# Optimization experiments

Hardware: AMD Instinct MI355X
Metric: run time of the kernel (lower is better)

## Reference

```python
import jax, jax.numpy as jnp
import numpy as np

MIN_, MAX_, KSZ, IGNORE_IDX = 10, 10, 3, -255
B, H, W = 256, 256, 256
LI_MAX_ITERS = 64


def setup_inputs() -> dict:
    key = jax.random.key(0)
    x = jax.random.uniform(key, (B, 1, H, W), dtype=jnp.float32)
    return {"x": x}


def _otsu(hist):
    # hist: [256] counts. Returns Otsu threshold (bin value); fg = img > t.
    bins = jnp.arange(256, dtype=jnp.float32)
    w0 = jnp.cumsum(hist)[:-1]
    w1 = hist.sum() - w0
    s0 = jnp.cumsum(hist * bins)[:-1]
    s_tot = (hist * bins).sum()
    m0 = s0 / jnp.maximum(w0, 1e-12)
    m1 = (s_tot - s0) / jnp.maximum(w1, 1e-12)
    var_b = w0 * w1 * (m0 - m1) ** 2
    return jnp.argmax(var_b).astype(jnp.float32)


def _li(hist, init_t):
    # Histogram-based Li iterative minimum cross-entropy threshold
    # (skimage.filters.threshold_li with initial_guess=init_t).
    bins = jnp.arange(256, dtype=jnp.float32)
    img_min = jnp.min(jnp.where(hist > 0, bins, 255.0))
    vals = bins - img_min  # shift so values >= 0 (as skimage does)
    csum = jnp.cumsum(hist)
    cvsum = jnp.cumsum(hist * vals)
    n_tot, s_tot = csum[-1], cvsum[-1]
    tol = 0.5  # integer image -> half the minimal value spacing

    def body(state):
        t_curr, _, i = state
        # background: img <= t_curr + img_min
        idx = jnp.clip(jnp.floor(t_curr + img_min).astype(jnp.int32), 0, 255)
        n_back, s_back = csum[idx], cvsum[idx]
        n_fore, s_fore = n_tot - n_back, s_tot - s_back
        mean_back = jnp.where(n_back > 0, s_back / jnp.maximum(n_back, 1.0), 0.0)
        mean_fore = s_fore / jnp.maximum(n_fore, 1.0)
        eps = 1e-12
        t_next = (mean_back - mean_fore) / (
            jnp.log(jnp.maximum(mean_back, eps)) - jnp.log(jnp.maximum(mean_fore, eps)))
        t_next = jnp.where(mean_back < eps, mean_fore / 2.0, t_next)
        return (t_next, t_curr, i + 1)

    def cond(state):
        t_curr, t_prev, i = state
        return (jnp.abs(t_curr - t_prev) > tol) & (i < LI_MAX_ITERS)

    t0 = init_t - img_min
    t_fin, _, _ = jax.lax.while_loop(cond, body, (t0, t0 + 10.0, 0))
    return t_fin + img_min


def _sample_mask(key, region, k):
    # Uniform sampling without replacement of up to k pixels from region
    # (bool [H,W]) via random-score top-k (equiv. to torch.multinomial
    # with uniform probs, w/o replacement).
    flat = region.reshape(-1)
    scores = jnp.where(flat, jax.random.uniform(key, (flat.shape[0],)), -1.0)
    top, idx = jax.lax.top_k(scores, k)
    valid = (top >= 0.0).astype(jnp.int32)
    mask = jnp.zeros(flat.shape[0], jnp.int32).at[idx].max(valid)
    return mask.reshape(region.shape)


def _dilate(m):
    # kornia dilation with ones (KSZ,KSZ) kernel on a 0/1 mask == max filter.
    return jax.lax.reduce_window(m, 0, jax.lax.max, (KSZ, KSZ), (1, 1), "SAME")


def _per_image(img_u8, key_fg, key_bg):
    # img_u8: [H,W] int32 in [0,255]
    hist = jnp.zeros(256, jnp.float32).at[img_u8.ravel()].add(1.0)
    otsu = jnp.clip(_otsu(hist), 1.0, 254.0)  # clamp 0->1, 255->254
    li_t = _li(hist, otsu)
    roi = img_u8.astype(jnp.float32) > li_t

    fg = _sample_mask(key_fg, roi, MAX_)
    bg = _sample_mask(key_bg, jnp.logical_not(roi), MIN_)
    if KSZ > 1:
        fg = _dilate(fg)
        bg = _dilate(bg)

    overlap = (fg + bg) == 2
    fg = jnp.where(overlap, 0, fg)
    bg = jnp.where(overlap, 0, bg)

    seeds = jnp.full((H, W), IGNORE_IDX, jnp.int32)
    seeds = jnp.where(bg == 1, 0, seeds)
    seeds = jnp.where(fg == 1, 1, seeds)
    return seeds


def reference(x):
    b = x.shape[0]
    # (cam*255).astype(uint8): truncation, cam in [0,1]
    img = jnp.clip(jnp.floor(x[:, 0] * 255.0), 0, 255).astype(jnp.int32)
    keys = jax.random.split(jax.random.key(1), (b, 2))
    return jax.vmap(_per_image)(img, keys[:, 0], keys[:, 1])
```

## Files before the change

kernel.cpp:

```cpp
#include <hip/hip_runtime.h>
#include <stdint.h>

#define NPIX 65536
#define IGN (-255)
#define CAP 768

__device__ __forceinline__ uint32_t rotl32(uint32_t v, uint32_t r){ return (v<<r)|(v>>(32u-r)); }

__device__ __forceinline__ void tf2x32(uint32_t k0, uint32_t k1, uint32_t x0, uint32_t x1,
                                       uint32_t &o0, uint32_t &o1){
  uint32_t k2 = k0 ^ k1 ^ 0x1BD11BDAu;
  x0 += k0; x1 += k1;
#define TFR(r) { x0 += x1; x1 = rotl32(x1,(r)); x1 ^= x0; }
  TFR(13u) TFR(15u) TFR(26u) TFR(6u)   x0 += k1; x1 += k2 + 1u;
  TFR(17u) TFR(29u) TFR(16u) TFR(24u)  x0 += k2; x1 += k0 + 2u;
  TFR(13u) TFR(15u) TFR(26u) TFR(6u)   x0 += k0; x1 += k1 + 3u;
  TFR(17u) TFR(29u) TFR(16u) TFR(24u)  x0 += k1; x1 += k2 + 4u;
  TFR(13u) TFR(15u) TFR(26u) TFR(6u)   x0 += k2; x1 += k0 + 5u;
#undef TFR
  o0 = x0; o1 = x1;
}

__device__ __forceinline__ void tf2_pair(uint32_t A0, uint32_t A1, uint32_t xA,
                                         uint32_t B0, uint32_t B1, uint32_t xB,
                                         uint32_t &rA, uint32_t &rB){
  uint32_t A2 = A0 ^ A1 ^ 0x1BD11BDAu;
  uint32_t B2 = B0 ^ B1 ^ 0x1BD11BDAu;
  uint32_t a0 = A0, a1 = xA + A1;
  uint32_t b0 = B0, b1 = xB + B1;
#define TFR2(r) { a0 += a1; b0 += b1; a1 = rotl32(a1,(r)); b1 = rotl32(b1,(r)); a1 ^= a0; b1 ^= b0; }
  TFR2(13u) TFR2(15u) TFR2(26u) TFR2(6u)
  a0 += A1; b0 += B1; a1 += A2 + 1u; b1 += B2 + 1u;
  TFR2(17u) TFR2(29u) TFR2(16u) TFR2(24u)
  a0 += A2; b0 += B2; a1 += A0 + 2u; b1 += B0 + 2u;
  TFR2(13u) TFR2(15u) TFR2(26u) TFR2(6u)
  a0 += A0; b0 += B0; a1 += A1 + 3u; b1 += B1 + 3u;
  TFR2(17u) TFR2(29u) TFR2(16u) TFR2(24u)
  a0 += A1; b0 += B1; a1 += A2 + 4u; b1 += B2 + 4u;
  TFR2(13u) TFR2(15u) TFR2(26u) TFR2(6u)
  a0 += A2; b0 += B2; a1 += A0 + 5u; b1 += B0 + 5u;
#undef TFR2
  rA = a0 ^ a1; rB = b0 ^ b1;
}

__device__ __forceinline__ unsigned long long packCand(uint32_t bits, uint32_t pix){
  float f = __uint_as_float((bits >> 9) | 0x3f800000u) - 1.0f;
  uint32_t u = __float_as_uint(f) ^ 0x80000000u;
  return ((unsigned long long)u << 32) | (unsigned long long)(0xFFFFFFFFu - pix);
}

__device__ __forceinline__ void t10_insert(unsigned long long* l, unsigned long long c){
  if (c > l[9]) {
    l[9] = c;
#pragma unroll
    for (int i = 9; i > 0; --i){
      unsigned long long a = l[i-1], b2 = l[i];
      if (b2 > a){ l[i-1] = b2; l[i] = a; }
    }
  }
}

__global__ __launch_bounds__(1024)
void apm_kernel(const float* __restrict__ x, int* __restrict__ out){
  const int b = blockIdx.x;
  const int tid = threadIdx.x;
  const float* img = x + (size_t)b * NPIX;
  int* outb = out + (size_t)b * NPIX;

  __shared__ uint32_t histR[1024];
  __shared__ float csum[256], cvsum[256];
  __shared__ uint32_t s_kw[4];
  __shared__ unsigned long long buf[2][CAP];
  __shared__ int s_cnt[2], s_fail[2], s_np[2];
  __shared__ int s_qthr, s_nroi;
  __shared__ unsigned long long s_top[2][64][10];
  __shared__ unsigned long long s_top2[2][8][10];
  __shared__ int s_pr[2][10], s_pc[2][10];

  histR[tid] = 0u;
  if (tid < 2){
    uint32_t o0, o1;
    tf2x32(0u, 1u, 0u, (uint32_t)(2*b + tid), o0, o1);
    s_kw[2*tid] = o0; s_kw[2*tid+1] = o1;
    s_cnt[tid] = 0;
  }
  __syncthreads();

  {
    const float4* x4 = (const float4*)img;
    int4* o4 = (int4*)outb;
    const int4 f4 = make_int4(IGN, IGN, IGN, IGN);
    const uint32_t c4 = (uint32_t)(tid & 3);
    for (int k = 0; k < 16; ++k){
      int i4 = tid + 1024*k;
      float4 v = x4[i4];
      uint32_t u0 = (uint32_t)min(max((int)floorf(v.x*255.0f),0),255);
      uint32_t u1 = (uint32_t)min(max((int)floorf(v.y*255.0f),0),255);
      uint32_t u2 = (uint32_t)min(max((int)floorf(v.z*255.0f),0),255);
      uint32_t u3 = (uint32_t)min(max((int)floorf(v.w*255.0f),0),255);
      outb[i4] = (int)(u0 | (u1<<8) | (u2<<16) | (u3<<24));
      if (i4 >= 4096) o4[i4] = f4;
      atomicAdd(&histR[(u0<<2)|c4],1u); atomicAdd(&histR[(u1<<2)|c4],1u);
      atomicAdd(&histR[(u2<<2)|c4],1u); atomicAdd(&histR[(u3<<2)|c4],1u);
    }
  }
  __syncthreads();

  if (tid < 64){
    const int lane = tid;
    const int4* hv = (const int4*)&histR[16*lane];
    int4 p0 = hv[0], p1 = hv[1], p2 = hv[2], p3 = hv[3];
    int h0 = p0.x + p0.y + p0.z + p0.w;
    int h1 = p1.x + p1.y + p1.z + p1.w;
    int h2 = p2.x + p2.y + p2.z + p2.w;
    int h3 = p3.x + p3.y + p3.z + p3.w;
    int cand = 256;
    if (h3) cand = 4*lane + 3;
    if (h2) cand = 4*lane + 2;
    if (h1) cand = 4*lane + 1;
    if (h0) cand = 4*lane + 0;
    for (int off = 32; off; off >>= 1) cand = min(cand, __shfl_xor(cand, off));
    const float img_min = (float)cand;
    float c0 = (float)h0, c1 = c0 + h1, c2 = c1 + h2, c3 = c2 + h3;
    float bv = 4.0f*lane - img_min;
    float v0 = h0*bv;
    float v1 = v0 + h1*(bv + 1.0f);
    float v2 = v1 + h2*(bv + 2.0f);
    float v3 = v2 + h3*(bv + 3.0f);
    float cc = c3, vv = v3;
    for (int off = 1; off < 64; off <<= 1){
      float a = __shfl_up(cc, off), b2 = __shfl_up(vv, off);
      if (lane >= off){ cc += a; vv += b2; }
    }
    const float cexc = cc - c3, vexc = vv - v3;
    const float cs0 = cexc+c0, cs1 = cexc+c1, cs2 = cexc+c2, cs3 = cexc+c3;
    const float vs0 = vexc+v0, vs1 = vexc+v1, vs2 = vexc+v2, vs3 = vexc+v3;
    csum[4*lane]   = cs0; csum[4*lane+1]  = cs1;
    csum[4*lane+2] = cs2; csum[4*lane+3]  = cs3;
    cvsum[4*lane]   = vs0; cvsum[4*lane+1] = vs1;
    cvsum[4*lane+2] = vs2; cvsum[4*lane+3] = vs3;
    const float ctot = __shfl(cc, 63), vtot = __shfl(vv, 63);
    const float s_tot_o = vtot + img_min * ctot;
    unsigned long long best = 0ull;
#define OTSU_BIN(CS, VS, J)                                              \
    { int bin = 4*lane + (J);                                            \
      if (bin < 255){                                                    \
        float w0_ = (CS);                                                \
        float w1_ = 65536.0f - w0_;                                      \
        float cs = (VS) + img_min * (CS);                                \
        float m0 = cs / fmaxf(w0_, 1e-12f);                              \
        float m1 = (s_tot_o - cs) / fmaxf(w1_, 1e-12f);                  \
        float d = m0 - m1;                                               \
        float vb = (w0_*w1_) * (d*d);                                    \
        unsigned long long pk =                                          \
          ((unsigned long long)__float_as_uint(vb) << 32) |              \
           (unsigned long long)(255 - bin);                              \
        if (pk > best) best = pk;                                        \
      } }
    OTSU_BIN(cs0, vs0, 0) OTSU_BIN(cs1, vs1, 1)
    OTSU_BIN(cs2, vs2, 2) OTSU_BIN(cs3, vs3, 3)
#undef OTSU_BIN
    for (int off = 32; off; off >>= 1){
      unsigned int hi = (unsigned int)(best >> 32), lo = (unsigned int)best;
      unsigned int hio = (unsigned int)__shfl_xor((int)hi, off);
      unsigned int loo = (unsigned int)__shfl_xor((int)lo, off);
      unsigned long long ob = ((unsigned long long)hio << 32) | loo;
      if (ob > best) best = ob;
    }
    if (lane == 0){
      int bestIdx = 255 - (int)(best & 0xFFFFFFFFull);
      float otsu = fminf(fmaxf((float)bestIdx, 1.0f), 254.0f);
      float n_tot = ctot, s_tot = vtot;
      float t_curr = otsu - img_min, t_prev = t_curr + 10.0f;
      int it = 0;
      while (fabsf(t_curr - t_prev) > 0.5f && it < 64){
        int idx = min(max((int)floorf(t_curr + img_min), 0), 255);
        float n_back = csum[idx], s_back = cvsum[idx];
        float n_fore = n_tot - n_back, s_fore = s_tot - s_back;
        float mean_back = (n_back > 0.0f) ? (s_back / fmaxf(n_back, 1.0f)) : 0.0f;
        float mean_fore = s_fore / fmaxf(n_fore, 1.0f);
        float t_next = (mean_back - mean_fore) /
                       (logf(fmaxf(mean_back, 1e-12f)) - logf(fmaxf(mean_fore, 1e-12f)));
        if (mean_back < 1e-12f) t_next = mean_fore * 0.5f;
        t_prev = t_curr; t_curr = t_next; ++it;
      }
      float lit = t_curr + img_min;
      int qthr;
      if (!(lit == lit)) qthr = 256;
      else               qthr = (int)floorf(lit) + 1;
      s_qthr = qthr;
      int nlo = (qthr <= 0) ? 0 : (int)csum[min(qthr, 256) - 1];
      s_nroi = NPIX - nlo;
    }
  }
  __syncthreads();

  const int qthr = s_qthr;
  const uint32_t fk0 = s_kw[0], fk1 = s_kw[1], bk0 = s_kw[2], bk1 = s_kw[3];
  const int4* u4 = (const int4*)outb;
  for (int k = 0; k < 4; ++k){
    int4 w = u4[tid + 1024*k];
    uint32_t pw0 = (uint32_t)(16*(tid + 1024*k));
#pragma unroll
    for (int m = 0; m < 4; ++m){
      uint32_t pk = (m==0)?(uint32_t)w.x:(m==1)?(uint32_t)w.y:(m==2)?(uint32_t)w.z:(uint32_t)w.w;
      uint32_t pb = pw0 + (uint32_t)(4*m);
#pragma unroll
      for (int h = 0; h < 2; ++h){
        int qa = (int)((pk >> (16*h))     & 255u);
        int qb = (int)((pk >> (16*h + 8)) & 255u);
        bool ra = (qa >= qthr), rb = (qb >= qthr);
        uint32_t pixA = pb + (uint32_t)(2*h), pixB = pixA + 1u;
        uint32_t bitsA, bitsB;
        tf2_pair(ra ? fk0 : bk0, ra ? fk1 : bk1, pixA,
                 rb ? fk0 : bk0, rb ? fk1 : bk1, pixB, bitsA, bitsB);
        if (bitsA >= 0xFF000000u){
          int r2 = ra ? 0 : 1;
          int idx = atomicAdd(&s_cnt[r2], 1);
          if (idx < CAP) buf[r2][idx] = packCand(bitsA, pixA);
        }
        if (bitsB >= 0xFF000000u){
          int r2 = rb ? 0 : 1;
          int idx = atomicAdd(&s_cnt[r2], 1);
          if (idx < CAP) buf[r2][idx] = packCand(bitsB, pixB);
        }
      }
    }
  }
  __syncthreads();

  if (tid < 2){
    int rs = tid ? (NPIX - s_nroi) : s_nroi;
    int cc = s_cnt[tid];
    s_fail[tid] = (cc > CAP) || (cc < 10 && cc != rs);
  }
  __syncthreads();

  const int wv = tid >> 6, lane = tid & 63;
  if (wv < 2){
    const int r2 = wv;
    unsigned long long t[10];
#pragma unroll
    for (int i = 0; i < 10; ++i) t[i] = 0ull;
    if (!s_fail[r2]){
      int n = min(s_cnt[r2], CAP);
      for (int i = lane; i < n; i += 64) t10_insert(t, buf[r2][i]);
    } else {
      const uint32_t kk0 = s_kw[2*r2], kk1 = s_kw[2*r2+1];
      for (int k = 0; k < 1024; ++k){
        uint32_t pix = (uint32_t)(lane + 64*k);
        int q = (int)(((uint32_t)outb[pix >> 2] >> (8*(pix & 3u))) & 255u);
        bool r = (q >= qthr);
        if (r == (r2 == 0)){
          uint32_t o0, o1; tf2x32(kk0, kk1, 0u, pix, o0, o1);
          t10_insert(t, packCand(o0 ^ o1, pix));
        }
      }
    }
#pragma unroll
    for (int i = 0; i < 10; ++i) s_top[r2][lane][i] = t[i];
  }
  __syncthreads();
  if (wv < 2 && lane < 8){
    unsigned long long t[10];
#pragma unroll
    for (int i = 0; i < 10; ++i) t[i] = 0ull;
    for (int l2 = 0; l2 < 8; ++l2)
#pragma unroll
      for (int i = 0; i < 10; ++i) t10_insert(t, s_top[wv][lane*8 + l2][i]);
#pragma unroll
    for (int i = 0; i < 10; ++i) s_top2[wv][lane][i] = t[i];
  }
  __syncthreads();
  if (wv < 2 && lane == 0){
    unsigned long long t[10];
#pragma unroll
    for (int i = 0; i < 10; ++i) t[i] = 0ull;
    for (int l2 = 0; l2 < 8; ++l2)
#pragma unroll
      for (int i = 0; i < 10; ++i) t10_insert(t, s_top2[wv][l2][i]);
    int np = 0;
    for (int i = 0; i < 10; ++i){
      if (t[i]){
        uint32_t pix = 0xFFFFFFFFu - (uint32_t)(t[i] & 0xFFFFFFFFull);
        s_pr[wv][np] = (int)(pix >> 8);
        s_pc[wv][np] = (int)(pix & 255u);
        ++np;
      }
    }
    s_np[wv] = np;
  }
  __syncthreads();

  {
    int4* o4 = (int4*)outb;
    const int4 f4 = make_int4(IGN, IGN, IGN, IGN);
#pragma unroll
    for (int k = 0; k < 4; ++k) o4[tid + 1024*k] = f4;
  }
  __syncthreads();

  const int nfg = s_np[0], nbg = s_np[1];
  const int npts = nfg + nbg;
  if (tid < npts*9){
    int k = tid / 9, d = tid - k*9;
    int pr = (k < nfg) ? s_pr[0][k] : s_pr[1][k - nfg];
    int pc = (k < nfg) ? s_pc[0][k] : s_pc[1][k - nfg];
    pr += d/3 - 1; pc += d%3 - 1;
    if (pr >= 0 && pr < 256 && pc >= 0 && pc < 256){
      bool fgd = false, bgd = false;
      for (int i = 0; i < nfg; ++i) fgd |= (abs(pr - s_pr[0][i]) <= 1) && (abs(pc - s_pc[0][i]) <= 1);
      for (int i = 0; i < nbg; ++i) bgd |= (abs(pr - s_pr[1][i]) <= 1) && (abs(pc - s_pc[1][i]) <= 1);
      int val = (fgd && bgd) ? IGN : (fgd ? 1 : 0);
      outb[pr*256 + pc] = val;
    }
  }
}

extern "C" void kernel_launch(void* const* d_in, const int* in_sizes, int n_in,
                              void* d_out, int out_size, void* d_ws, size_t ws_size,
                              hipStream_t stream) {
  const float* x = (const float*)d_in[0];
  int* out = (int*)d_out;
  int B = in_sizes[0] / NPIX;
  apm_kernel<<<B, 1024, 0, stream>>>(x, out);
}
```

Before: 172.7 us.

## Keep packed u8 image in LDS instead of scratch-staging it in output buffer

Stores the quantized 8-bit packed image in a 64KB shared-memory array instead of writing it into the first quarter of the global output and reading it back. The output is filled with the ignore value once during the load phase, which removes the later global refill pass and one barrier. Input loads are batched eight float4s at a time to raise memory-level parallelism. The extra 64KB of LDS per block pushes total shared memory to roughly 100KB, which may limit blocks per CU.

```diff
diff --git a/kernel.cpp b/kernel.cpp
--- a/kernel.cpp
+++ b/kernel.cpp
@@ -67,6 +67,7 @@
   const float* img = x + (size_t)b * NPIX;
   int* outb = out + (size_t)b * NPIX;
 
+  __shared__ uint32_t u8img[16384];
   __shared__ uint32_t histR[1024];
   __shared__ float csum[256], cvsum[256];
   __shared__ uint32_t s_kw[4];
@@ -91,18 +92,29 @@
     int4* o4 = (int4*)outb;
     const int4 f4 = make_int4(IGN, IGN, IGN, IGN);
     const uint32_t c4 = (uint32_t)(tid & 3);
-    for (int k = 0; k < 16; ++k){
-      int i4 = tid + 1024*k;
-      float4 v = x4[i4];
-      uint32_t u0 = (uint32_t)min(max((int)floorf(v.x*255.0f),0),255);
-      uint32_t u1 = (uint32_t)min(max((int)floorf(v.y*255.0f),0),255);
-      uint32_t u2 = (uint32_t)min(max((int)floorf(v.z*255.0f),0),255);
-      uint32_t u3 = (uint32_t)min(max((int)floorf(v.w*255.0f),0),255);
-      outb[i4] = (int)(u0 | (u1<<8) | (u2<<16) | (u3<<24));
-      if (i4 >= 4096) o4[i4] = f4;
-      atomicAdd(&histR[(u0<<2)|c4],1u); atomicAdd(&histR[(u1<<2)|c4],1u);
-      atomicAdd(&histR[(u2<<2)|c4],1u); atomicAdd(&histR[(u3<<2)|c4],1u);
-    }
+#define PROC(V, K) {                                                          \
+      uint32_t u0 = (uint32_t)min(max((int)floorf((V).x*255.0f),0),255);      \
+      uint32_t u1 = (uint32_t)min(max((int)floorf((V).y*255.0f),0),255);      \
+      uint32_t u2 = (uint32_t)min(max((int)floorf((V).z*255.0f),0),255);      \
+      uint32_t u3 = (uint32_t)min(max((int)floorf((V).w*255.0f),0),255);      \
+      u8img[tid + 1024*(K)] = u0 | (u1<<8) | (u2<<16) | (u3<<24);             \
+      o4[tid + 1024*(K)] = f4;                                                \
+      atomicAdd(&histR[(u0<<2)|c4],1u); atomicAdd(&histR[(u1<<2)|c4],1u);     \
+      atomicAdd(&histR[(u2<<2)|c4],1u); atomicAdd(&histR[(u3<<2)|c4],1u); }
+    for (int kk = 0; kk < 2; ++kk){
+      int base = 8*kk;
+      float4 v0 = x4[tid + 1024*(base+0)];
+      float4 v1 = x4[tid + 1024*(base+1)];
+      float4 v2 = x4[tid + 1024*(base+2)];
+      float4 v3 = x4[tid + 1024*(base+3)];
+      float4 v4 = x4[tid + 1024*(base+4)];
+      float4 v5 = x4[tid + 1024*(base+5)];
+      float4 v6 = x4[tid + 1024*(base+6)];
+      float4 v7 = x4[tid + 1024*(base+7)];
+      PROC(v0, base+0) PROC(v1, base+1) PROC(v2, base+2) PROC(v3, base+3)
+      PROC(v4, base+4) PROC(v5, base+5) PROC(v6, base+6) PROC(v7, base+7)
+    }
+#undef PROC
   }
   __syncthreads();
 
@@ -197,7 +209,7 @@
 
   const int qthr = s_qthr;
   const uint32_t fk0 = s_kw[0], fk1 = s_kw[1], bk0 = s_kw[2], bk1 = s_kw[3];
-  const int4* u4 = (const int4*)outb;
+  const int4* u4 = (const int4*)u8img;
   for (int k = 0; k < 4; ++k){
     int4 w = u4[tid + 1024*k];
     uint32_t pw0 = (uint32_t)(16*(tid + 1024*k));
@@ -249,7 +261,7 @@
       const uint32_t kk0 = s_kw[2*r2], kk1 = s_kw[2*r2+1];
       for (int k = 0; k < 1024; ++k){
         uint32_t pix = (uint32_t)(lane + 64*k);
-        int q = (int)(((uint32_t)outb[pix >> 2] >> (8*(pix & 3u))) & 255u);
+        int q = (int)((u8img[pix >> 2] >> (8*(pix & 3u))) & 255u);
         bool r = (q >= qthr);
         if (r == (r2 == 0)){
           uint32_t o0, o1; tf2x32(kk0, kk1, 0u, pix, o0, o1);
@@ -289,14 +301,6 @@
       }
     }
     s_np[wv] = np;
-  }
-  __syncthreads();
-
-  {
-    int4* o4 = (int4*)outb;
-    const int4 f4 = make_int4(IGN, IGN, IGN, IGN);
-#pragma unroll
-    for (int k = 0; k < 4; ++k) o4[tid + 1024*k] = f4;
   }
   __syncthreads();
 
```

Measured after the change: 173.1 us. Within noise of the previous version (+0.2%).
